# Performance work log

Hardware: AMD Instinct MI355X
Metric: run time of the kernel (lower is better)

The kernel has to match this reference:

```python
import jax, jax.numpy as jnp
import numpy as np

B, S, H, E, TOPK = 8, 512, 1024, 8, 2


def setup_inputs() -> dict:
    key = jax.random.key(0)
    ks = jax.random.split(key, 10)
    D = 2 * H
    inp = {
        "vector": jax.random.normal(ks[0], (B, S, D), dtype=jnp.float32),
        # gate weights (Linear(H, E)): stored as [H, E] for x @ W + b
        "Wg": jax.random.normal(ks[1], (H, E), dtype=jnp.float32) * 0.02,
        "bg": jnp.zeros((E,), dtype=jnp.float32),
        "Wf": jax.random.normal(ks[2], (H, E), dtype=jnp.float32) * 0.02,
        "bf": jnp.zeros((E,), dtype=jnp.float32),
        # expert MLP weights, stacked over experts: Linear(2H,2H) -> ReLU -> Linear(2H,2H)
        "W1": jax.random.normal(ks[3], (E, D, D), dtype=jnp.float32) * 0.02,
        "b1": jnp.zeros((E, D), dtype=jnp.float32),
        "W2": jax.random.normal(ks[4], (E, D, D), dtype=jnp.float32) * 0.02,
        "b2": jnp.zeros((E, D), dtype=jnp.float32),
        # combine weights (config['initializer_weight'])
        "weight": jnp.ones((2,), dtype=jnp.float32),
        "top_k": TOPK,
    }
    return inp


def reference(vector, Wg, bg, Wf, bf, W1, b1, W2, b2, weight, top_k):
    h = Wg.shape[0]
    n_exp = Wg.shape[1]
    # gate_g on first half, softmax, then top-k sparsify (scatter of topk values)
    rout_g = jax.nn.softmax(vector[:, :, :h] @ Wg + bg, axis=-1)           # [B,S,E]
    vals, idx = jax.lax.top_k(rout_g, top_k)                               # [B,S,k]
    route_g = jnp.sum(jax.nn.one_hot(idx, n_exp, dtype=vals.dtype) * vals[..., None], axis=-2)  # [B,S,E]
    # gate_f on second half: dense softmax routing
    rout_f = jax.nn.softmax(vector[:, :, h:2 * h] @ Wf + bf, axis=-1)      # [B,S,E]
    # dense expert computation for every token (dropout = identity at eval)
    hidden = jax.nn.relu(jnp.einsum('bsd,edh->bseh', vector, W1) + b1)     # [B,S,E,2H]
    expert_out = jnp.einsum('bseh,ehd->bsed', hidden, W2) + b2             # [B,S,E,2H]
    out0 = weight[0] * jnp.einsum('bsed,bse->bsd', expert_out[..., :h], route_g)
    out1 = weight[1] * jnp.einsum('bsed,bse->bsd', expert_out[..., h:2 * h], rout_f)
    return (out0, out1)
```

## Files before the change

### kernel.cpp

```cpp
#include <hip/hip_runtime.h>

#define TOKENS 4096
#define DDIM   2048
#define HDIM   1024
#define NEXP   8
#define GK     2048
#define GN     2048

typedef __bf16 bf16_t;
typedef __bf16 bf16x8 __attribute__((ext_vector_type(8)));
typedef __bf16 bf16x4 __attribute__((ext_vector_type(4)));
typedef float  f32x4  __attribute__((ext_vector_type(4)));

__device__ inline void gld_lds16(const bf16_t* g, bf16_t* l) {
  __builtin_amdgcn_global_load_lds(
      (const __attribute__((address_space(1))) void*)g,
      (__attribute__((address_space(3))) void*)l, 16, 0, 0);
}

#define VMC(n)  asm volatile("s_waitcnt vmcnt(" #n ")" ::: "memory")
#define BAR()   __builtin_amdgcn_s_barrier()

__global__ __launch_bounds__(256)
void k_routing(const float* __restrict__ vec,
               const float* __restrict__ Wg, const float* __restrict__ bg,
               const float* __restrict__ Wf, const float* __restrict__ bfv,
               const float* __restrict__ wgt,
               float* __restrict__ c0, float* __restrict__ c1)
{
  const int wave = threadIdx.x >> 6;
  const int lane = threadIdx.x & 63;
  const int m = blockIdx.x * 4 + wave;
  const float* v = vec + (size_t)m * DDIM;

  float ag[NEXP], af[NEXP];
#pragma unroll
  for (int e = 0; e < NEXP; ++e) { ag[e] = 0.f; af[e] = 0.f; }

  for (int i = lane; i < HDIM; i += 64) {
    const float xg = v[i];
    const float xf = v[HDIM + i];
    const float4 wg0 = *(const float4*)(Wg + i * NEXP);
    const float4 wg1 = *(const float4*)(Wg + i * NEXP + 4);
    const float4 wf0 = *(const float4*)(Wf + i * NEXP);
    const float4 wf1 = *(const float4*)(Wf + i * NEXP + 4);
    ag[0] += xg * wg0.x; ag[1] += xg * wg0.y; ag[2] += xg * wg0.z; ag[3] += xg * wg0.w;
    ag[4] += xg * wg1.x; ag[5] += xg * wg1.y; ag[6] += xg * wg1.z; ag[7] += xg * wg1.w;
    af[0] += xf * wf0.x; af[1] += xf * wf0.y; af[2] += xf * wf0.z; af[3] += xf * wf0.w;
    af[4] += xf * wf1.x; af[5] += xf * wf1.y; af[6] += xf * wf1.z; af[7] += xf * wf1.w;
  }
#pragma unroll
  for (int e = 0; e < NEXP; ++e) {
#pragma unroll
    for (int off = 32; off >= 1; off >>= 1) {
      ag[e] += __shfl_xor(ag[e], off, 64);
      af[e] += __shfl_xor(af[e], off, 64);
    }
  }
  if (lane == 0) {
    float g[NEXP], f[NEXP];
    float mg = -1e30f, mf = -1e30f;
#pragma unroll
    for (int e = 0; e < NEXP; ++e) {
      g[e] = ag[e] + bg[e]; mg = fmaxf(mg, g[e]);
      f[e] = af[e] + bfv[e]; mf = fmaxf(mf, f[e]);
    }
    float sg = 0.f, sf = 0.f;
#pragma unroll
    for (int e = 0; e < NEXP; ++e) {
      g[e] = expf(g[e] - mg); sg += g[e];
      f[e] = expf(f[e] - mf); sf += f[e];
    }
    const float rg = 1.f / sg, rf = 1.f / sf;
#pragma unroll
    for (int e = 0; e < NEXP; ++e) { g[e] *= rg; f[e] *= rf; }
    int i1 = 0;
#pragma unroll
    for (int e = 1; e < NEXP; ++e) if (g[e] > g[i1]) i1 = e;
    int i2 = (i1 == 0) ? 1 : 0;
#pragma unroll
    for (int e = 0; e < NEXP; ++e) if (e != i1 && g[e] > g[i2]) i2 = e;
    const float w0 = wgt[0], w1 = wgt[1];
#pragma unroll
    for (int e = 0; e < NEXP; ++e) {
      c0[e * TOKENS + m] = (e == i1 || e == i2) ? w0 * g[e] : 0.f;
      c1[e * TOKENS + m] = w1 * f[e];
    }
  }
}

__global__ __launch_bounds__(256)
void k_cvt(const float* __restrict__ in, bf16_t* __restrict__ out)
{
  const size_t i = ((size_t)blockIdx.x * 256 + threadIdx.x) * 8;
  const float4 a = *(const float4*)(in + i);
  const float4 b = *(const float4*)(in + i + 4);
  bf16x8 o;
  o[0] = (bf16_t)a.x; o[1] = (bf16_t)a.y; o[2] = (bf16_t)a.z; o[3] = (bf16_t)a.w;
  o[4] = (bf16_t)b.x; o[5] = (bf16_t)b.y; o[6] = (bf16_t)b.z; o[7] = (bf16_t)b.w;
  *(bf16x8*)(out + i) = o;
}

#define TP 68
__global__ __launch_bounds__(256)
void k_cvt_wt(const float* __restrict__ W, bf16_t* __restrict__ Wt)
{
  __shared__ __attribute__((aligned(16))) bf16_t tile[64 * TP];
  const size_t eoff = (size_t)blockIdx.z * DDIM * DDIM;
  const float* w = W + eoff;
  bf16_t* wt = Wt + eoff;
  const int k0 = blockIdx.x * 64;
  const int n0 = blockIdx.y * 64;
  const int t = threadIdx.x;
  const int c4 = (t & 15) * 4;
  const int rb = (t >> 4) * 4;
#pragma unroll
  for (int rr = 0; rr < 4; ++rr) {
    const int r = rb + rr;
    const float4 v = *(const float4*)(w + (size_t)(k0 + r) * DDIM + n0 + c4);
    tile[(c4 + 0) * TP + r] = (bf16_t)v.x;
    tile[(c4 + 1) * TP + r] = (bf16_t)v.y;
    tile[(c4 + 2) * TP + r] = (bf16_t)v.z;
    tile[(c4 + 3) * TP + r] = (bf16_t)v.w;
  }
  __syncthreads();
  const int nl = t >> 2;
  const int kq = (t & 3) * 16;
  bf16_t* dst = wt + (size_t)(n0 + nl) * DDIM + k0 + kq;
#pragma unroll
  for (int j2 = 0; j2 < 4; ++j2) {
    bf16x4 u = *(const bf16x4*)(&tile[nl * TP + kq + j2 * 4]);
    *(bf16x4*)(dst + j2 * 4) = u;
  }
}


#define FRG(base, R, KQ) \
  (*(const bf16x8*)((base) + ((((R) * 32 + (KQ)) ^ ((((R) >> 3) & 1) << 4)))))

#define MFMA_(d, x, y) (d) = __builtin_amdgcn_mfma_f32_16x16x32_bf16((x), (y), (d), 0, 0, 0)

__global__ __launch_bounds__(512, 2)
void k_gemm1_8p(const bf16_t* __restrict__ A, const bf16_t* __restrict__ W1t,
                const float* __restrict__ b1, bf16_t* __restrict__ Hd)
{
  __shared__ __attribute__((aligned(16))) bf16_t AsF[4 * 8192];
  __shared__ __attribute__((aligned(16))) bf16_t BsF[4 * 8192];
  const int e = blockIdx.z;
  const int t = threadIdx.x;
  const int wave = t >> 6, lane = t & 63;
  const int m0 = blockIdx.x * 256, n0 = blockIdx.y * 256;
  const int wm = (wave >> 2) * 128, wn = (wave & 3) * 64;
  const int fr = lane & 15, kq = (lane >> 4) * 8;

  const int sRw = wave * 16 + (lane >> 2);
  const int sC  = ((lane & 3) * 8) ^ (((lane >> 5) & 1) << 4);
  const bf16_t* aSrc = A + (size_t)(m0 + sRw) * GK + sC;
  const bf16_t* bSrc = W1t + (size_t)e * GN * GK + (size_t)(n0 + sRw) * GK + sC;
  bf16_t* aDst = AsF + wave * 512;
  bf16_t* bDst = BsF + wave * 512;

#define STG1(P, U) do { const bf16_t* _sa = aSrc + (size_t)(P) * 32; \
    const bf16_t* _sb = bSrc + (size_t)(P) * 32; \
    gld_lds16(_sa, aDst + (U) * 8192); \
    gld_lds16(_sa + (size_t)128 * GK, aDst + (U) * 8192 + 4096); \
    gld_lds16(_sb, bDst + (U) * 8192); \
    gld_lds16(_sb + (size_t)128 * GK, bDst + (U) * 8192 + 4096); } while (0)

  f32x4 acc[8][4] = {};
  bf16x8 fAa[8], fAb[4], fBa[8], fBb[4];

#define RD1(SET, U) do { \
    _Pragma("unroll") \
    for (int _j = 0; _j < 4; ++_j) SET##b[_j] = FRG(BsF + (U) * 8192, wn + _j * 16 + fr, kq); \
    _Pragma("unroll") \
    for (int _i = 0; _i < 8; ++_i) SET##a[_i] = FRG(AsF + (U) * 8192, wm + _i * 16 + fr, kq); \
  } while (0)

#define MM1(SET) do { \
    __builtin_amdgcn_s_setprio(1); \
    _Pragma("unroll") \
    for (int _i = 0; _i < 8; ++_i) \
      _Pragma("unroll") \
      for (int _j = 0; _j < 4; ++_j) MFMA_(acc[_i][_j], SET##a[_i], SET##b[_j]); \
    __builtin_amdgcn_s_setprio(0); \
  } while (0)

  STG1(0, 0); STG1(1, 1); STG1(2, 2);
  VMC(4); BAR();
  RD1(fA, 0);

#pragma unroll 1
  for (int pb = 0; pb < 56; pb += 4) {
    STG1(pb + 3, 3); RD1(fB, 1); MM1(fA); VMC(4); BAR();
    STG1(pb + 4, 0); RD1(fA, 2); MM1(fB); VMC(4); BAR();
    STG1(pb + 5, 1); RD1(fB, 3); MM1(fA); VMC(4); BAR();
    STG1(pb + 6, 2); RD1(fA, 0); MM1(fB); VMC(4); BAR();
  }
  STG1(59, 3); RD1(fB, 1); MM1(fA); VMC(4); BAR();
  STG1(60, 0); RD1(fA, 2); MM1(fB); VMC(4); BAR();
  STG1(61, 1); RD1(fB, 3); MM1(fA); VMC(4); BAR();
  STG1(62, 2); RD1(fA, 0); MM1(fB); VMC(4); BAR();
  STG1(63, 3); RD1(fB, 1); MM1(fA); VMC(4); BAR();
  RD1(fA, 2); MM1(fB); VMC(0); BAR();
  RD1(fB, 3); MM1(fA); BAR();
  MM1(fB);

  const float* bias = b1 + (size_t)e * DDIM;
  bf16_t* Hb = Hd + (size_t)e * TOKENS * DDIM;
  const int ecol = lane & 15, erow = (lane >> 4) * 4;
#pragma unroll
  for (int j = 0; j < 4; ++j) {
    const int gn = n0 + wn + j * 16 + ecol;
    const float bv = bias[gn];
#pragma unroll
    for (int i = 0; i < 8; ++i) {
      const int gm = m0 + wm + i * 16 + erow;
#pragma unroll
      for (int r = 0; r < 4; ++r) {
        float v = acc[i][j][r] + bv;
        v = v > 0.f ? v : 0.f;
        Hb[(size_t)(gm + r) * DDIM + gn] = (bf16_t)v;
      }
    }
  }
#undef RD1
#undef MM1
#undef STG1
}

__global__ __launch_bounds__(512, 2)
void k_gemm2_8p(const bf16_t* __restrict__ Hd, const bf16_t* __restrict__ W2t,
                const float* __restrict__ b2,
                const float* __restrict__ c0, const float* __restrict__ c1,
                float* __restrict__ out0, float* __restrict__ out1)
{
  __shared__ __attribute__((aligned(16))) bf16_t AsF[4 * 4096];
  __shared__ __attribute__((aligned(16))) bf16_t BsF[4 * 8192];
  __shared__ float cs[NEXP][128];
  __shared__ float bsh[NEXP][256];

  const int t = threadIdx.x;
  const int wave = t >> 6, lane = t & 63;
  const int m0 = blockIdx.x * 128, n0 = blockIdx.y * 256;
  const int wm = (wave >> 2) * 64, wn = (wave & 3) * 64;
  const int fr = lane & 15, kq = (lane >> 4) * 8;
  const bool hi = (n0 >= HDIM);
  const float* cc = hi ? c1 : c0;

  for (int idx = t; idx < NEXP * 128; idx += 512) {
    const int ee = idx >> 7, r = idx & 127;
    cs[ee][r] = cc[ee * TOKENS + m0 + r];
  }
  for (int idx = t; idx < NEXP * 256; idx += 512) {
    const int ee = idx >> 8, r = idx & 255;
    bsh[ee][r] = b2[ee * DDIM + n0 + r];
  }
  __syncthreads();

  const int sRw = wave * 16 + (lane >> 2);
  const int sC  = ((lane & 3) * 8) ^ (((lane >> 5) & 1) << 4);
  const bf16_t* aSrc = Hd + (size_t)(m0 + sRw) * GK + sC;
  const bf16_t* bSrc = W2t + (size_t)(n0 + sRw) * GK + sC;
  bf16_t* aDst = AsF + wave * 512;
  bf16_t* bDst = BsF + wave * 512;

#define STG2(P, U) do { \
    const bf16_t* _sa = aSrc + (size_t)((P) >> 6) * ((size_t)TOKENS * GK) + (size_t)((P) & 63) * 32; \
    const bf16_t* _sb = bSrc + (size_t)((P) >> 6) * ((size_t)GN * GK) + (size_t)((P) & 63) * 32; \
    gld_lds16(_sa, aDst + (U) * 4096); \
    gld_lds16(_sb, bDst + (U) * 8192); \
    gld_lds16(_sb + (size_t)128 * GK, bDst + (U) * 8192 + 4096); } while (0)

  f32x4 acc[4][4] = {};
  f32x4 fin[4][4] = {};
  bf16x8 fAa[4], fAb[4], fBa[4], fBb[4];

#define RD2(SET, U) do { \
    _Pragma("unroll") \
    for (int _j = 0; _j < 4; ++_j) SET##b[_j] = FRG(BsF + (U) * 8192, wn + _j * 16 + fr, kq); \
    _Pragma("unroll") \
    for (int _i = 0; _i < 4; ++_i) SET##a[_i] = FRG(AsF + (U) * 4096, wm + _i * 16 + fr, kq); \
  } while (0)

#define MM2(SET) do { \
    __builtin_amdgcn_s_setprio(1); \
    _Pragma("unroll") \
    for (int _i = 0; _i < 4; ++_i) \
      _Pragma("unroll") \
      for (int _j = 0; _j < 4; ++_j) MFMA_(acc[_i][_j], SET##a[_i], SET##b[_j]); \
    __builtin_amdgcn_s_setprio(0); \
  } while (0)

  const int ecol = lane & 15, erow = (lane >> 4) * 4;

#define FOLD2(E) do { \
    _Pragma("unroll") \
    for (int _j = 0; _j < 4; ++_j) { \
      const float _bv = bsh[E][wn + _j * 16 + ecol]; \
      _Pragma("unroll") \
      for (int _i = 0; _i < 4; ++_i) { \
        const int _rw = wm + _i * 16 + erow; \
        _Pragma("unroll") \
        for (int _r = 0; _r < 4; ++_r) { \
          fin[_i][_j][_r] += cs[E][_rw + _r] * (acc[_i][_j][_r] + _bv); \
          acc[_i][_j][_r] = 0.f; \
        } \
      } \
    } \
  } while (0)

  STG2(0, 0); STG2(1, 1); STG2(2, 2);
  VMC(3); BAR();
  RD2(fA, 0);

#pragma unroll 1
  for (int pb = 0; pb < 504; pb += 4) {
    STG2(pb + 3, 3); RD2(fB, 1); MM2(fA); VMC(3); BAR();
    STG2(pb + 4, 0); RD2(fA, 2); MM2(fB); VMC(3); BAR();
    STG2(pb + 5, 1); RD2(fB, 3); MM2(fA); VMC(3); BAR();
    STG2(pb + 6, 2); RD2(fA, 0); MM2(fB);
    if (((pb + 3) & 63) == 63) FOLD2((pb + 3) >> 6);
    VMC(3); BAR();
  }
  STG2(507, 3); RD2(fB, 1); MM2(fA); VMC(3); BAR();
  STG2(508, 0); RD2(fA, 2); MM2(fB); VMC(3); BAR();
  STG2(509, 1); RD2(fB, 3); MM2(fA); VMC(3); BAR();
  STG2(510, 2); RD2(fA, 0); MM2(fB); VMC(3); BAR();
  STG2(511, 3); RD2(fB, 1); MM2(fA); VMC(3); BAR();
  RD2(fA, 2); MM2(fB); VMC(0); BAR();
  RD2(fB, 3); MM2(fA); BAR();
  MM2(fB);
  FOLD2(7);

#pragma unroll
  for (int j = 0; j < 4; ++j) {
    const int gn = n0 + wn + j * 16 + ecol;
    float* ob = hi ? (out1 + (gn - HDIM)) : (out0 + gn);
#pragma unroll
    for (int i = 0; i < 4; ++i) {
      const int gm = m0 + wm + i * 16 + erow;
#pragma unroll
      for (int r = 0; r < 4; ++r)
        ob[(size_t)(gm + r) * HDIM] = fin[i][j][r];
    }
  }
#undef RD2
#undef MM2
#undef STG2
#undef FOLD2
}

__global__ __launch_bounds__(256, 2)
void k_gemm_relu(const bf16_t* __restrict__ A, const bf16_t* __restrict__ W1t,
                 const float* __restrict__ b1, bf16_t* __restrict__ Hd)
{
  __shared__ __attribute__((aligned(16))) bf16_t As[128 * 32];
  __shared__ __attribute__((aligned(16))) bf16_t Bs[128 * 32];
  const int e = blockIdx.z;
  const bf16_t* Bt = W1t + (size_t)e * GK * GN;
  const float* bias = b1 + (size_t)e * GN;
  bf16_t* H = Hd + (size_t)e * TOKENS * GN;

  const int t = threadIdx.x;
  const int wave = t >> 6;
  const int lane = t & 63;
  const int m0 = blockIdx.x * 128;
  const int n0 = blockIdx.y * 128;
  const int wm = (wave >> 1) << 6;
  const int wn = (wave & 1) << 6;

  f32x4 acc[4][4] = {};

  const bf16_t* aP0 = A + (size_t)(m0 + (t >> 2)) * GK + (t & 3) * 8;
  const bf16_t* aP1 = aP0 + (size_t)64 * GK;
  const bf16_t* bP0 = Bt + (size_t)(n0 + (t >> 2)) * GK + (t & 3) * 8;
  const bf16_t* bP1 = bP0 + (size_t)64 * GK;
  bf16_t* lA0 = As + wave * 512;
  bf16_t* lA1 = As + 2048 + wave * 512;
  bf16_t* lB0 = Bs + wave * 512;
  bf16_t* lB1 = Bs + 2048 + wave * 512;

  const int fr = lane & 15;
  const int kq = (lane >> 4) * 8;

  for (int k0 = 0; k0 < GK; k0 += 32) {
    gld_lds16(aP0 + k0, lA0);
    gld_lds16(aP1 + k0, lA1);
    gld_lds16(bP0 + k0, lB0);
    gld_lds16(bP1 + k0, lB1);
    __syncthreads();
    bf16x8 afr[4], bfr[4];
#pragma unroll
    for (int i = 0; i < 4; ++i) {
      afr[i] = *(const bf16x8*)(As + (wm + i * 16 + fr) * 32 + kq);
      bfr[i] = *(const bf16x8*)(Bs + (wn + i * 16 + fr) * 32 + kq);
    }
#pragma unroll
    for (int i = 0; i < 4; ++i)
#pragma unroll
      for (int j = 0; j < 4; ++j)
        acc[i][j] = __builtin_amdgcn_mfma_f32_16x16x32_bf16(afr[i], bfr[j], acc[i][j], 0, 0, 0);
    __syncthreads();
  }

  const int col = lane & 15;
  const int rq  = (lane >> 4) * 4;
#pragma unroll
  for (int j = 0; j < 4; ++j) {
    const int gn = n0 + wn + j * 16 + col;
    const float bv = bias[gn];
#pragma unroll
    for (int i = 0; i < 4; ++i) {
      const int gm = m0 + wm + i * 16 + rq;
#pragma unroll
      for (int r = 0; r < 4; ++r) {
        float v = acc[i][j][r] + bv;
        v = v > 0.f ? v : 0.f;
        H[(size_t)(gm + r) * GN + gn] = (bf16_t)v;
      }
    }
  }
}

__global__ __launch_bounds__(256, 2)
void k_gemm_out(const bf16_t* __restrict__ A, const bf16_t* __restrict__ Bt,
                const float* __restrict__ bias,
                const float* __restrict__ c0, const float* __restrict__ c1,
                float* __restrict__ out0, float* __restrict__ out1, const int accum)
{
  __shared__ __attribute__((aligned(16))) bf16_t As[128 * 32];
  __shared__ __attribute__((aligned(16))) bf16_t Bs[128 * 32];
  const int t = threadIdx.x;
  const int wave = t >> 6;
  const int lane = t & 63;
  const int m0 = blockIdx.x * 128;
  const int n0 = blockIdx.y * 128;
  const int wm = (wave >> 1) << 6;
  const int wn = (wave & 1) << 6;

  f32x4 acc[4][4] = {};

  const bf16_t* aP0 = A + (size_t)(m0 + (t >> 2)) * GK + (t & 3) * 8;
  const bf16_t* aP1 = aP0 + (size_t)64 * GK;
  const bf16_t* bP0 = Bt + (size_t)(n0 + (t >> 2)) * GK + (t & 3) * 8;
  const bf16_t* bP1 = bP0 + (size_t)64 * GK;
  bf16_t* lA0 = As + wave * 512;
  bf16_t* lA1 = As + 2048 + wave * 512;
  bf16_t* lB0 = Bs + wave * 512;
  bf16_t* lB1 = Bs + 2048 + wave * 512;

  const int fr = lane & 15;
  const int kq = (lane >> 4) * 8;

  for (int k0 = 0; k0 < GK; k0 += 32) {
    gld_lds16(aP0 + k0, lA0);
    gld_lds16(aP1 + k0, lA1);
    gld_lds16(bP0 + k0, lB0);
    gld_lds16(bP1 + k0, lB1);
    __syncthreads();
    bf16x8 afr[4], bfr[4];
#pragma unroll
    for (int i = 0; i < 4; ++i) {
      afr[i] = *(const bf16x8*)(As + (wm + i * 16 + fr) * 32 + kq);
      bfr[i] = *(const bf16x8*)(Bs + (wn + i * 16 + fr) * 32 + kq);
    }
#pragma unroll
    for (int i = 0; i < 4; ++i)
#pragma unroll
      for (int j = 0; j < 4; ++j)
        acc[i][j] = __builtin_amdgcn_mfma_f32_16x16x32_bf16(afr[i], bfr[j], acc[i][j], 0, 0, 0);
    __syncthreads();
  }

  const int col = lane & 15;
  const int rq  = (lane >> 4) * 4;
#pragma unroll
  for (int j = 0; j < 4; ++j) {
    const int gn = n0 + wn + j * 16 + col;
    const float bv = bias[gn];
    const bool lo = gn < HDIM;
    float* obase = lo ? (out0 + gn) : (out1 + (gn - HDIM));
    const float* cc = lo ? c0 : c1;
#pragma unroll
    for (int i = 0; i < 4; ++i) {
      const int gmB = m0 + wm + i * 16 + rq;
#pragma unroll
      for (int r = 0; r < 4; ++r) {
        const int gm = gmB + r;
        float v = (acc[i][j][r] + bv) * cc[gm];
        float* dst = obase + (size_t)gm * HDIM;
        if (accum) v += *dst;
        *dst = v;
      }
    }
  }
}

extern "C" void kernel_launch(void* const* d_in, const int* in_sizes, int n_in,
                              void* d_out, int out_size, void* d_ws, size_t ws_size,
                              hipStream_t stream)
{
  const float* vec = (const float*)d_in[0];
  const float* Wg  = (const float*)d_in[1];
  const float* bg  = (const float*)d_in[2];
  const float* Wf  = (const float*)d_in[3];
  const float* bfv = (const float*)d_in[4];
  const float* W1  = (const float*)d_in[5];
  const float* b1  = (const float*)d_in[6];
  const float* W2  = (const float*)d_in[7];
  const float* b2  = (const float*)d_in[8];
  const float* wgt = (const float*)d_in[9];

  float* out0 = (float*)d_out;
  float* out1 = out0 + (size_t)TOKENS * HDIM;

  char* base = (char*)d_ws;
  const size_t XB = (size_t)TOKENS * DDIM * 2;
  const size_t HB = (size_t)NEXP * TOKENS * DDIM * 2;
  const size_t WT = (size_t)NEXP * DDIM * DDIM * 2;

  bf16_t* Xbf = (bf16_t*)base;
  float*  c0  = (float*)(base + XB);
  float*  c1  = c0 + (size_t)NEXP * TOKENS;
  size_t off = XB + 2 * (size_t)NEXP * TOKENS * 4;

  k_routing<<<dim3(TOKENS / 4), 256, 0, stream>>>(vec, Wg, bg, Wf, bfv, wgt, c0, c1);
  k_cvt<<<dim3((TOKENS * DDIM) / 2048), 256, 0, stream>>>(vec, Xbf);

  if (ws_size >= off + HB + 2 * WT) {
    bf16_t* hidden = (bf16_t*)(base + off);
    bf16_t* W1t    = (bf16_t*)(base + off + HB);
    bf16_t* W2t    = (bf16_t*)(base + off + HB + WT);
    k_cvt_wt<<<dim3(32, 32, NEXP), 256, 0, stream>>>(W1, W1t);
    k_cvt_wt<<<dim3(32, 32, NEXP), 256, 0, stream>>>(W2, W2t);
    k_gemm1_8p<<<dim3(16, 8, NEXP), 512, 0, stream>>>(Xbf, W1t, b1, hidden);
    k_gemm2_8p<<<dim3(32, 8), 512, 0, stream>>>(hidden, W2t, b2, c0, c1, out0, out1);
  } else {
    bf16_t* hidden = (bf16_t*)(base + off);
    bf16_t* W1t    = hidden + (size_t)TOKENS * DDIM;
    bf16_t* W2t    = W1t + (size_t)DDIM * DDIM;
    for (int e = 0; e < NEXP; ++e) {
      k_cvt_wt<<<dim3(32, 32, 1), 256, 0, stream>>>(W1 + (size_t)e * DDIM * DDIM, W1t);
      k_cvt_wt<<<dim3(32, 32, 1), 256, 0, stream>>>(W2 + (size_t)e * DDIM * DDIM, W2t);
      k_gemm_relu<<<dim3(32, 16, 1), 256, 0, stream>>>(Xbf, W1t, b1 + (size_t)e * DDIM, hidden);
      k_gemm_out<<<dim3(32, 16), 256, 0, stream>>>(
          hidden, W2t, b2 + (size_t)e * DDIM,
          c0 + (size_t)e * TOKENS, c1 + (size_t)e * TOKENS, out0, out1, e > 0);
    }
  }
}
```

Before: 1.064 ms.

## Halve barriers in MoE GEMM pipelines with two k-steps per sync and deeper LDS rings

Restructures the software pipelines of both expert GEMM kernels so each barrier covers two 32-wide k-steps instead of one. GEMM1 gets decoupled A (4-slot) and B (5-slot) LDS rings with a rotating slot schedule, and GEMM2 gets 6-slot rings for both operands. Both kernels drop the double-buffered register fragment sets, which lowers VGPR pressure. The aim is less barrier and wait overhead per MFMA. In exchange LDS use grows, which may limit occupancy at 2 blocks per CU, and the hand-written slot schedules are fragile.

Result: faster. 1.019 ms (-4.2%).

```diff
diff --git a/kernel.cpp b/kernel.cpp
--- a/kernel.cpp
+++ b/kernel.cpp
@@ -145,7 +145,7 @@
                 const float* __restrict__ b1, bf16_t* __restrict__ Hd)
 {
   __shared__ __attribute__((aligned(16))) bf16_t AsF[4 * 8192];
-  __shared__ __attribute__((aligned(16))) bf16_t BsF[4 * 8192];
+  __shared__ __attribute__((aligned(16))) bf16_t BsF[5 * 8192];
   const int e = blockIdx.z;
   const int t = threadIdx.x;
   const int wave = t >> 6, lane = t & 63;
@@ -160,51 +160,63 @@
   bf16_t* aDst = AsF + wave * 512;
   bf16_t* bDst = BsF + wave * 512;
 
-#define STG1(P, U) do { const bf16_t* _sa = aSrc + (size_t)(P) * 32; \
-    const bf16_t* _sb = bSrc + (size_t)(P) * 32; \
-    gld_lds16(_sa, aDst + (U) * 8192); \
-    gld_lds16(_sa + (size_t)128 * GK, aDst + (U) * 8192 + 4096); \
-    gld_lds16(_sb, bDst + (U) * 8192); \
-    gld_lds16(_sb + (size_t)128 * GK, bDst + (U) * 8192 + 4096); } while (0)
+#define STGA1(P, U) do { const bf16_t* _s = aSrc + (size_t)(P) * 32; \
+    gld_lds16(_s, aDst + (U) * 8192); \
+    gld_lds16(_s + (size_t)128 * GK, aDst + (U) * 8192 + 4096); } while (0)
+#define STGB1(P, U) do { const bf16_t* _s = bSrc + (size_t)(P) * 32; \
+    gld_lds16(_s, bDst + (U) * 8192); \
+    gld_lds16(_s + (size_t)128 * GK, bDst + (U) * 8192 + 4096); } while (0)
 
   f32x4 acc[8][4] = {};
-  bf16x8 fAa[8], fAb[4], fBa[8], fBb[4];
-
-#define RD1(SET, U) do { \
-    _Pragma("unroll") \
-    for (int _j = 0; _j < 4; ++_j) SET##b[_j] = FRG(BsF + (U) * 8192, wn + _j * 16 + fr, kq); \
-    _Pragma("unroll") \
-    for (int _i = 0; _i < 8; ++_i) SET##a[_i] = FRG(AsF + (U) * 8192, wm + _i * 16 + fr, kq); \
+  bf16x8 a_[8], b_[4];
+
+#define RD1(UA, UB) do { \
+    _Pragma("unroll") \
+    for (int _j = 0; _j < 4; ++_j) b_[_j] = FRG(BsF + (UB) * 8192, wn + _j * 16 + fr, kq); \
+    _Pragma("unroll") \
+    for (int _i = 0; _i < 8; ++_i) a_[_i] = FRG(AsF + (UA) * 8192, wm + _i * 16 + fr, kq); \
   } while (0)
 
-#define MM1(SET) do { \
+#define MM1() do { \
     __builtin_amdgcn_s_setprio(1); \
     _Pragma("unroll") \
     for (int _i = 0; _i < 8; ++_i) \
       _Pragma("unroll") \
-      for (int _j = 0; _j < 4; ++_j) MFMA_(acc[_i][_j], SET##a[_i], SET##b[_j]); \
+      for (int _j = 0; _j < 4; ++_j) MFMA_(acc[_i][_j], a_[_i], b_[_j]); \
     __builtin_amdgcn_s_setprio(0); \
   } while (0)
 
-  STG1(0, 0); STG1(1, 1); STG1(2, 2);
-  VMC(4); BAR();
-  RD1(fA, 0);
+#define G1(a0, b0, a1, b1, pA2, uA2, pA3, uA3, pB3, uB3, pB4, uB4) do { \
+    RD1(a0, b0); \
+    STGA1(pA2, uA2); STGA1(pA3, uA3); STGB1(pB3, uB3); STGB1(pB4, uB4); \
+    MM1(); \
+    RD1(a1, b1); MM1(); \
+    VMC(2); BAR(); \
+  } while (0)
+
+  STGA1(0, 0); STGA1(1, 1);
+  STGB1(0, 0); STGB1(1, 1); STGB1(2, 2);
+  VMC(2); BAR();
 
 #pragma unroll 1
-  for (int pb = 0; pb < 56; pb += 4) {
-    STG1(pb + 3, 3); RD1(fB, 1); MM1(fA); VMC(4); BAR();
-    STG1(pb + 4, 0); RD1(fA, 2); MM1(fB); VMC(4); BAR();
-    STG1(pb + 5, 1); RD1(fB, 3); MM1(fA); VMC(4); BAR();
-    STG1(pb + 6, 2); RD1(fA, 0); MM1(fB); VMC(4); BAR();
-  }
-  STG1(59, 3); RD1(fB, 1); MM1(fA); VMC(4); BAR();
-  STG1(60, 0); RD1(fA, 2); MM1(fB); VMC(4); BAR();
-  STG1(61, 1); RD1(fB, 3); MM1(fA); VMC(4); BAR();
-  STG1(62, 2); RD1(fA, 0); MM1(fB); VMC(4); BAR();
-  STG1(63, 3); RD1(fB, 1); MM1(fA); VMC(4); BAR();
-  RD1(fA, 2); MM1(fB); VMC(0); BAR();
-  RD1(fB, 3); MM1(fA); BAR();
-  MM1(fB);
+  for (int it = 0; it < 3; ++it) {
+    const int P = it * 20;
+    G1(0, 0, 1, 1,  P + 2, 2,  P + 3, 3,  P + 3, 3,  P + 4, 4);
+    G1(2, 2, 3, 3,  P + 4, 0,  P + 5, 1,  P + 5, 0,  P + 6, 1);
+    G1(0, 4, 1, 0,  P + 6, 2,  P + 7, 3,  P + 7, 2,  P + 8, 3);
+    G1(2, 1, 3, 2,  P + 8, 0,  P + 9, 1,  P + 9, 4,  P + 10, 0);
+    G1(0, 3, 1, 4,  P + 10, 2, P + 11, 3, P + 11, 1, P + 12, 2);
+    G1(2, 0, 3, 1,  P + 12, 0, P + 13, 1, P + 13, 3, P + 14, 4);
+    G1(0, 2, 1, 3,  P + 14, 2, P + 15, 3, P + 15, 0, P + 16, 1);
+    G1(2, 4, 3, 0,  P + 16, 0, P + 17, 1, P + 17, 2, P + 18, 3);
+    G1(0, 1, 1, 2,  P + 18, 2, P + 19, 3, P + 19, 4, P + 20, 0);
+    G1(2, 3, 3, 4,  P + 20, 0, P + 21, 1, P + 21, 1, P + 22, 2);
+  }
+  RD1(0, 0); STGA1(62, 2); STGA1(63, 3); STGB1(63, 3); MM1();
+  RD1(1, 1); MM1();
+  VMC(0); BAR();
+  RD1(2, 2); MM1();
+  RD1(3, 3); MM1();
 
   const float* bias = b1 + (size_t)e * DDIM;
   bf16_t* Hb = Hd + (size_t)e * TOKENS * DDIM;
@@ -226,7 +238,9 @@
   }
 #undef RD1
 #undef MM1
-#undef STG1
+#undef G1
+#undef STGA1
+#undef STGB1
 }
 
 __global__ __launch_bounds__(512, 2)
@@ -235,8 +249,8 @@
                 const float* __restrict__ c0, const float* __restrict__ c1,
                 float* __restrict__ out0, float* __restrict__ out1)
 {
-  __shared__ __attribute__((aligned(16))) bf16_t AsF[4 * 4096];
-  __shared__ __attribute__((aligned(16))) bf16_t BsF[4 * 8192];
+  __shared__ __attribute__((aligned(16))) bf16_t AsF[6 * 4096];
+  __shared__ __attribute__((aligned(16))) bf16_t BsF[6 * 8192];
   __shared__ float cs[NEXP][128];
   __shared__ float bsh[NEXP][256];
 
@@ -274,21 +288,21 @@
 
   f32x4 acc[4][4] = {};
   f32x4 fin[4][4] = {};
-  bf16x8 fAa[4], fAb[4], fBa[4], fBb[4];
-
-#define RD2(SET, U) do { \
-    _Pragma("unroll") \
-    for (int _j = 0; _j < 4; ++_j) SET##b[_j] = FRG(BsF + (U) * 8192, wn + _j * 16 + fr, kq); \
-    _Pragma("unroll") \
-    for (int _i = 0; _i < 4; ++_i) SET##a[_i] = FRG(AsF + (U) * 4096, wm + _i * 16 + fr, kq); \
+  bf16x8 a_[4], b_[4];
+
+#define RD2(U) do { \
+    _Pragma("unroll") \
+    for (int _j = 0; _j < 4; ++_j) b_[_j] = FRG(BsF + (U) * 8192, wn + _j * 16 + fr, kq); \
+    _Pragma("unroll") \
+    for (int _i = 0; _i < 4; ++_i) a_[_i] = FRG(AsF + (U) * 4096, wm + _i * 16 + fr, kq); \
   } while (0)
 
-#define MM2(SET) do { \
+#define MM2() do { \
     __builtin_amdgcn_s_setprio(1); \
     _Pragma("unroll") \
     for (int _i = 0; _i < 4; ++_i) \
       _Pragma("unroll") \
-      for (int _j = 0; _j < 4; ++_j) MFMA_(acc[_i][_j], SET##a[_i], SET##b[_j]); \
+      for (int _j = 0; _j < 4; ++_j) MFMA_(acc[_i][_j], a_[_i], b_[_j]); \
     __builtin_amdgcn_s_setprio(0); \
   } while (0)
 
@@ -310,27 +324,22 @@
     } \
   } while (0)
 
-  STG2(0, 0); STG2(1, 1); STG2(2, 2);
-  VMC(3); BAR();
-  RD2(fA, 0);
+#define FCHK(G) do { if ((((G) + 1) & 31) == 0) FOLD2((G) >> 5); } while (0)
+
+  STG2(0, 0); STG2(1, 1); STG2(2, 2); STG2(3, 3);
+  VMC(6); BAR();
 
 #pragma unroll 1
-  for (int pb = 0; pb < 504; pb += 4) {
-    STG2(pb + 3, 3); RD2(fB, 1); MM2(fA); VMC(3); BAR();
-    STG2(pb + 4, 0); RD2(fA, 2); MM2(fB); VMC(3); BAR();
-    STG2(pb + 5, 1); RD2(fB, 3); MM2(fA); VMC(3); BAR();
-    STG2(pb + 6, 2); RD2(fA, 0); MM2(fB);
-    if (((pb + 3) & 63) == 63) FOLD2((pb + 3) >> 6);
-    VMC(3); BAR();
-  }
-  STG2(507, 3); RD2(fB, 1); MM2(fA); VMC(3); BAR();
-  STG2(508, 0); RD2(fA, 2); MM2(fB); VMC(3); BAR();
-  STG2(509, 1); RD2(fB, 3); MM2(fA); VMC(3); BAR();
-  STG2(510, 2); RD2(fA, 0); MM2(fB); VMC(3); BAR();
-  STG2(511, 3); RD2(fB, 1); MM2(fA); VMC(3); BAR();
-  RD2(fA, 2); MM2(fB); VMC(0); BAR();
-  RD2(fB, 3); MM2(fA); BAR();
-  MM2(fB);
+  for (int it = 0; it < 84; ++it) {
+    const int P = it * 6, g0 = it * 3;
+    RD2(0); STG2(P + 4, 4); STG2(P + 5, 5); MM2(); RD2(1); MM2(); FCHK(g0);     VMC(6); BAR();
+    RD2(2); STG2(P + 6, 0); STG2(P + 7, 1); MM2(); RD2(3); MM2(); FCHK(g0 + 1); VMC(6); BAR();
+    RD2(4); STG2(P + 8, 2); STG2(P + 9, 3); MM2(); RD2(5); MM2(); FCHK(g0 + 2); VMC(6); BAR();
+  }
+  RD2(0); STG2(508, 4); STG2(509, 5); MM2(); RD2(1); MM2(); VMC(6); BAR();
+  RD2(2); STG2(510, 0); STG2(511, 1); MM2(); RD2(3); MM2(); VMC(6); BAR();
+  RD2(4); MM2(); RD2(5); MM2(); VMC(0); BAR();
+  RD2(0); MM2(); RD2(1); MM2();
   FOLD2(7);
 
 #pragma unroll
@@ -349,6 +358,7 @@
 #undef MM2
 #undef STG2
 #undef FOLD2
+#undef FCHK
 }
 
 __global__ __launch_bounds__(256, 2)
```
